# Performance work log

Measured on AMD Instinct MI355X. Metric: run time of the kernel, lower is better.

Reference implementation:

```python
import jax, jax.numpy as jnp
import numpy as np
import math

B, T, D, H, FFN_DIM, SE_HID = 16, 1024, 512, 8, 2048, 256
EPS = 1e-5  # torch LayerNorm default


def layer_norm(x, g, b):
    mu = jnp.mean(x, axis=-1, keepdims=True)
    var = jnp.mean((x - mu) ** 2, axis=-1, keepdims=True)
    return (x - mu) * jax.lax.rsqrt(var + EPS) * g + b


def setup_inputs() -> dict:
    key = jax.random.key(0)
    ks = jax.random.split(key, 8)
    s = 0.02
    return {
        "x": jax.random.normal(ks[0], (B, T, D), dtype=jnp.float32),
        "wq": jax.random.normal(ks[1], (D, D), dtype=jnp.float32) * s,
        "wk": jax.random.normal(ks[2], (D, D), dtype=jnp.float32) * s,
        "wv": jax.random.normal(ks[3], (D, D), dtype=jnp.float32) * s,
        "ln1_g": jnp.ones((D,), jnp.float32),
        "ln1_b": jnp.zeros((D,), jnp.float32),
        "se_w1": jax.random.normal(ks[4], (T, SE_HID), dtype=jnp.float32) * s,
        "se_w2": jax.random.normal(ks[5], (SE_HID, T), dtype=jnp.float32) * s,
        "ffn_g": jnp.ones((D,), jnp.float32),
        "ffn_b": jnp.zeros((D,), jnp.float32),
        "w1": jax.random.normal(ks[6], (D, FFN_DIM), dtype=jnp.float32) * s,
        "b1": jnp.zeros((FFN_DIM,), jnp.float32),
        "w2": jax.random.normal(ks[7], (FFN_DIM, D), dtype=jnp.float32) * s,
        "b2": jnp.zeros((D,), jnp.float32),
    }


def _forward(x, wq, wk, wv, ln1_g, ln1_b, se_w1, se_w2, ffn_g, ffn_b, w1, b1, w2, b2):
    # --- SE gate over the sequence axis: squeeze over feature dim D ---
    y = jnp.mean(x, axis=-1)                       # (B, T)
    gate = jax.nn.sigmoid(jax.nn.relu(y @ se_w1) @ se_w2)  # (B, T)
    x = x + x * gate[..., None]

    d = D // H
    n = layer_norm(x, ln1_g, ln1_b)
    q = (n @ wq).reshape(B, T, H, d)
    k = (n @ wk).reshape(B, T, H, d)
    v = (n @ wv).reshape(B, T, H, d)
    attn = jnp.einsum('bnhd,bmhd->bnmh', q, k) / math.sqrt(d)
    w = jax.nn.softmax(attn, axis=2)               # softmax over key dim m
    x = x + jnp.einsum('bnmh,bmhd->bnhd', w, v).reshape(B, T, D)

    # --- FFN (pre-norm, exact GELU as nn.GELU default) ---
    n2 = layer_norm(x, ffn_g, ffn_b)
    h = jax.nn.gelu(n2 @ w1 + b1, approximate=False)
    return x + (h @ w2 + b2)


def reference(x, wq, wk, wv, ln1_g, ln1_b, se_w1, se_w2, ffn_g, ffn_b, w1, b1, w2, b2):
    return _forward(x, wq, wk, wv, ln1_g, ln1_b, se_w1, se_w2, ffn_g, ffn_b, w1, b1, w2, b2)
```

## Files before the change

kernel.cpp:

```cpp
#include <hip/hip_runtime.h>

typedef unsigned int uint32;

using bf16x8 = __attribute__((ext_vector_type(8))) short;
using f32x4  = __attribute__((ext_vector_type(4))) float;

#define B_  16
#define T_  1024
#define D_  512
#define H_  8
#define HD_ 64
#define FFN_ 2048
#define SEH_ 256
#define EPS_ 1e-5f
#define PS_ 80

__device__ __forceinline__ ushort f2bf(float f) {
  uint32 x = __float_as_uint(f);
  return (ushort)((x + 0x7fffu + ((x >> 16) & 1u)) >> 16);
}
__device__ __forceinline__ float bf2f(ushort u) {
  return __uint_as_float(((uint32)u) << 16);
}
__device__ __forceinline__ float gelu_fast(float v) {
  float u = v * (0.7978845608f + 0.0356774081f * v * v);
  float e = __expf(2.0f * u);
  float t = 1.0f - 2.0f * __builtin_amdgcn_rcpf(e + 1.0f);
  return 0.5f * v * (1.0f + t);
}

__global__ __launch_bounds__(256) void cast_transpose_all_k(
    const float* __restrict__ wq, const float* __restrict__ wk,
    const float* __restrict__ wv, const float* __restrict__ w1,
    const float* __restrict__ w2, ushort* __restrict__ wqkvT,
    ushort* __restrict__ w1T, ushort* __restrict__ w2T) {
  __shared__ float tile[32][33];
  int bid = blockIdx.x;
  const float* W; ushort* WT; int K, N, bk, bn;
  if (bid < 768) {
    int w = bid >> 8, r = bid & 255;
    W = (w == 0) ? wq : (w == 1) ? wk : wv;
    WT = wqkvT + (size_t)w * 512 * 512;
    K = 512; N = 512; bk = (r >> 4) * 32; bn = (r & 15) * 32;
  } else if (bid < 1792) {
    int r = bid - 768;
    W = w1; WT = w1T; K = 512; N = 2048; bk = (r >> 6) * 32; bn = (r & 63) * 32;
  } else {
    int r = bid - 1792;
    W = w2; WT = w2T; K = 2048; N = 512; bk = (r >> 4) * 32; bn = (r & 15) * 32;
  }
  int lx = threadIdx.x & 31;
  int ly = threadIdx.x >> 5;
  #pragma unroll
  for (int i = ly; i < 32; i += 8)
    tile[i][lx] = W[(size_t)(bk + i) * N + bn + lx];
  __syncthreads();
  #pragma unroll
  for (int i = ly; i < 32; i += 8)
    WT[(size_t)(bn + i) * K + bk + lx] = f2bf(tile[lx][i]);
}

__global__ __launch_bounds__(256) void se_rowmean_k(const float* __restrict__ x,
                                                    float* __restrict__ y) {
  int row  = blockIdx.x * 4 + (threadIdx.x >> 6);
  int lane = threadIdx.x & 63;
  const float4* p = (const float4*)(x + (size_t)row * D_);
  float4 a = p[lane * 2];
  float4 b = p[lane * 2 + 1];
  float s = a.x + a.y + a.z + a.w + b.x + b.y + b.z + b.w;
  #pragma unroll
  for (int m = 1; m < 64; m <<= 1) s += __shfl_xor(s, m);
  if (lane == 0) y[row] = s * (1.0f / D_);
}

__global__ __launch_bounds__(256) void se_mlp1_k(const float* __restrict__ y,
                                                 const float* __restrict__ w1,
                                                 float* __restrict__ z) {
  __shared__ float yb[T_];
  __shared__ float part[8][32];
  int b = blockIdx.x, jt = blockIdx.y;
  int tid = threadIdx.x;
  #pragma unroll
  for (int i = 0; i < 4; i++) yb[tid + i * 256] = y[(size_t)b * T_ + tid + i * 256];
  __syncthreads();
  int tj = tid & 31, tk = tid >> 5;
  int j = jt * 32 + tj;
  const float* wp = w1 + (size_t)(tk * 128) * SEH_ + j;
  const float* yp = yb + tk * 128;
  float a0 = 0.f, a1 = 0.f, a2 = 0.f, a3 = 0.f;
  #pragma unroll
  for (int t = 0; t < 128; t += 4) {
    a0 += yp[t]     * wp[(t)     * SEH_];
    a1 += yp[t + 1] * wp[(t + 1) * SEH_];
    a2 += yp[t + 2] * wp[(t + 2) * SEH_];
    a3 += yp[t + 3] * wp[(t + 3) * SEH_];
  }
  part[tk][tj] = (a0 + a1) + (a2 + a3);
  __syncthreads();
  if (tid < 32) {
    float s = 0.f;
    #pragma unroll
    for (int k = 0; k < 8; k++) s += part[k][tid];
    z[(size_t)b * SEH_ + jt * 32 + tid] = fmaxf(s, 0.f);
  }
}

__global__ __launch_bounds__(256) void se_mlp2_k(const float* __restrict__ z,
                                                 const float* __restrict__ w2,
                                                 float* __restrict__ gate) {
  __shared__ float zb[SEH_];
  __shared__ float part[2][128];
  int b = blockIdx.x, bt = blockIdx.y;
  int tid = threadIdx.x;
  zb[tid & 255] = z[(size_t)b * SEH_ + (tid & 255)];
  __syncthreads();
  int tt = tid & 127, tk = tid >> 7;
  int t = bt * 128 + tt;
  const float* wp = w2 + (size_t)(tk * 128) * T_ + t;
  const float* zp = zb + tk * 128;
  float a0 = 0.f, a1 = 0.f, a2 = 0.f, a3 = 0.f;
  #pragma unroll
  for (int j = 0; j < 128; j += 4) {
    a0 += zp[j]     * wp[(j)     * T_];
    a1 += zp[j + 1] * wp[(j + 1) * T_];
    a2 += zp[j + 2] * wp[(j + 2) * T_];
    a3 += zp[j + 3] * wp[(j + 3) * T_];
  }
  part[tk][tt] = (a0 + a1) + (a2 + a3);
  __syncthreads();
  if (tid < 128) {
    float s = part[0][tid] + part[1][tid];
    gate[(size_t)b * T_ + bt * 128 + tid] = 1.0f / (1.0f + __expf(-s));
  }
}

__global__ __launch_bounds__(256) void gate_ln1_k(
    const float* __restrict__ x, const float* __restrict__ gate,
    const float* __restrict__ g, const float* __restrict__ beta,
    float* __restrict__ x1, ushort* __restrict__ nbuf) {
  int rid  = blockIdx.x * 4 + (threadIdx.x >> 6);
  int lane = threadIdx.x & 63;
  const float4* xr = (const float4*)(x + (size_t)rid * D_);
  float4 a = xr[lane * 2];
  float4 b = xr[lane * 2 + 1];
  float gv = 1.0f + gate[rid];
  a.x *= gv; a.y *= gv; a.z *= gv; a.w *= gv;
  b.x *= gv; b.y *= gv; b.z *= gv; b.w *= gv;
  float4* x1r = (float4*)(x1 + (size_t)rid * D_);
  x1r[lane * 2]     = a;
  x1r[lane * 2 + 1] = b;
  float s  = a.x + a.y + a.z + a.w + b.x + b.y + b.z + b.w;
  float ss = a.x*a.x + a.y*a.y + a.z*a.z + a.w*a.w + b.x*b.x + b.y*b.y + b.z*b.z + b.w*b.w;
  #pragma unroll
  for (int m = 1; m < 64; m <<= 1) { s += __shfl_xor(s, m); ss += __shfl_xor(ss, m); }
  float mu   = s * (1.0f / D_);
  float var  = ss * (1.0f / D_) - mu * mu;
  float rstd = rsqrtf(var + EPS_);
  const float4* gp = (const float4*)g;
  const float4* bp = (const float4*)beta;
  float4 g0 = gp[lane * 2], g1 = gp[lane * 2 + 1];
  float4 b0 = bp[lane * 2], b1 = bp[lane * 2 + 1];
  union { uint4 v; ushort u[8]; } pk;
  pk.u[0] = f2bf((a.x - mu) * rstd * g0.x + b0.x);
  pk.u[1] = f2bf((a.y - mu) * rstd * g0.y + b0.y);
  pk.u[2] = f2bf((a.z - mu) * rstd * g0.z + b0.z);
  pk.u[3] = f2bf((a.w - mu) * rstd * g0.w + b0.w);
  pk.u[4] = f2bf((b.x - mu) * rstd * g1.x + b1.x);
  pk.u[5] = f2bf((b.y - mu) * rstd * g1.y + b1.y);
  pk.u[6] = f2bf((b.z - mu) * rstd * g1.z + b1.z);
  pk.u[7] = f2bf((b.w - mu) * rstd * g1.w + b1.w);
  *(uint4*)(nbuf + (size_t)rid * D_ + lane * 8) = pk.v;
}

__global__ __launch_bounds__(256) void ln2_k(
    const float* __restrict__ x2, const float* __restrict__ g,
    const float* __restrict__ beta, ushort* __restrict__ nbuf) {
  int rid  = blockIdx.x * 4 + (threadIdx.x >> 6);
  int lane = threadIdx.x & 63;
  const float4* xr = (const float4*)(x2 + (size_t)rid * D_);
  float4 a = xr[lane * 2];
  float4 b = xr[lane * 2 + 1];
  float s  = a.x + a.y + a.z + a.w + b.x + b.y + b.z + b.w;
  float ss = a.x*a.x + a.y*a.y + a.z*a.z + a.w*a.w + b.x*b.x + b.y*b.y + b.z*b.z + b.w*b.w;
  #pragma unroll
  for (int m = 1; m < 64; m <<= 1) { s += __shfl_xor(s, m); ss += __shfl_xor(ss, m); }
  float mu   = s * (1.0f / D_);
  float var  = ss * (1.0f / D_) - mu * mu;
  float rstd = rsqrtf(var + EPS_);
  const float4* gp = (const float4*)g;
  const float4* bp = (const float4*)beta;
  float4 g0 = gp[lane * 2], g1 = gp[lane * 2 + 1];
  float4 b0 = bp[lane * 2], b1 = bp[lane * 2 + 1];
  union { uint4 v; ushort u[8]; } pk;
  pk.u[0] = f2bf((a.x - mu) * rstd * g0.x + b0.x);
  pk.u[1] = f2bf((a.y - mu) * rstd * g0.y + b0.y);
  pk.u[2] = f2bf((a.z - mu) * rstd * g0.z + b0.z);
  pk.u[3] = f2bf((a.w - mu) * rstd * g0.w + b0.w);
  pk.u[4] = f2bf((b.x - mu) * rstd * g1.x + b1.x);
  pk.u[5] = f2bf((b.y - mu) * rstd * g1.y + b1.y);
  pk.u[6] = f2bf((b.z - mu) * rstd * g1.z + b1.z);
  pk.u[7] = f2bf((b.w - mu) * rstd * g1.w + b1.w);
  *(uint4*)(nbuf + (size_t)rid * D_ + lane * 8) = pk.v;
}

__global__ __launch_bounds__(256) void gemm128_k(
    const ushort* __restrict__ A, const ushort* __restrict__ BT,
    int M, int N, int K,
    const float* __restrict__ bias, const float* __restrict__ resid,
    ushort* __restrict__ outB, ushort* __restrict__ outB2,
    ushort* __restrict__ vTout, float* __restrict__ outF, int epi) {
  __shared__ ushort As[128 * 32];
  __shared__ ushort Bs[128 * 32];
  int tid  = threadIdx.x;
  int wave = tid >> 6;
  int lane = tid & 63;
  int quad = lane >> 4;
  int l15  = lane & 15;
  int wm   = wave >> 1;
  int wn   = wave & 1;
  int m0 = blockIdx.x * 128;
  int n0 = blockIdx.y * 128;

  f32x4 acc[4][4];
  #pragma unroll
  for (int mt = 0; mt < 4; mt++)
    #pragma unroll
    for (int nt = 0; nt < 4; nt++) acc[mt][nt] = (f32x4){0.f, 0.f, 0.f, 0.f};

  int lrow = lane >> 2;
  int lcol = (lane & 3) * 8;

  const ushort* Ag = A  + (size_t)(m0 + wave * 32 + lrow) * K + lcol;
  const ushort* Bg = BT + (size_t)(n0 + wave * 32 + lrow) * K + lcol;
  ushort* AsW = As + (wave * 32) * 32;
  ushort* BsW = Bs + (wave * 32) * 32;

  for (int kk = 0; kk < K; kk += 32) {
    __builtin_amdgcn_global_load_lds(
        (const __attribute__((address_space(1))) void*)(Ag + kk),
        (__attribute__((address_space(3))) void*)AsW, 16, 0, 0);
    __builtin_amdgcn_global_load_lds(
        (const __attribute__((address_space(1))) void*)(Ag + kk + 16 * (size_t)K),
        (__attribute__((address_space(3))) void*)(AsW + 16 * 32), 16, 0, 0);
    __builtin_amdgcn_global_load_lds(
        (const __attribute__((address_space(1))) void*)(Bg + kk),
        (__attribute__((address_space(3))) void*)BsW, 16, 0, 0);
    __builtin_amdgcn_global_load_lds(
        (const __attribute__((address_space(1))) void*)(Bg + kk + 16 * (size_t)K),
        (__attribute__((address_space(3))) void*)(BsW + 16 * 32), 16, 0, 0);
    __syncthreads();
    bf16x8 af[4], bfr[4];
    #pragma unroll
    for (int mt = 0; mt < 4; mt++)
      af[mt] = *(const bf16x8*)(As + (wm * 64 + mt * 16 + l15) * 32 + quad * 8);
    #pragma unroll
    for (int nt = 0; nt < 4; nt++)
      bfr[nt] = *(const bf16x8*)(Bs + (wn * 64 + nt * 16 + l15) * 32 + quad * 8);
    #pragma unroll
    for (int mt = 0; mt < 4; mt++)
      #pragma unroll
      for (int nt = 0; nt < 4; nt++)
        acc[mt][nt] = __builtin_amdgcn_mfma_f32_16x16x32_bf16(af[mt], bfr[nt], acc[mt][nt], 0, 0, 0);
    __syncthreads();
  }

  if (epi == 1) {
    #pragma unroll
    for (int nt = 0; nt < 4; nt++) {
      int n = n0 + wn * 64 + nt * 16 + l15;
      float bv = bias[n];
      #pragma unroll
      for (int mt = 0; mt < 4; mt++) {
        #pragma unroll
        for (int r = 0; r < 4; r++) {
          int m = m0 + wm * 64 + mt * 16 + quad * 4 + r;
          outB[(size_t)m * N + n] = f2bf(gelu_fast(acc[mt][nt][r] + bv));
        }
      }
    }
  } else if (epi == 2) {
    #pragma unroll
    for (int nt = 0; nt < 4; nt++) {
      int n = n0 + wn * 64 + nt * 16 + l15;
      float bv = bias[n];
      #pragma unroll
      for (int mt = 0; mt < 4; mt++) {
        #pragma unroll
        for (int r = 0; r < 4; r++) {
          int m = m0 + wm * 64 + mt * 16 + quad * 4 + r;
          size_t idx = (size_t)m * N + n;
          outF[idx] = acc[mt][nt][r] + bv + resid[idx];
        }
      }
    }
  } else {
    if (n0 < 1024) {
      ushort* dst = (n0 < 512) ? outB : outB2;
      float scl = (n0 < 512) ? 0.125f : 1.0f;
      int nb = n0 & 511;
      #pragma unroll
      for (int nt = 0; nt < 4; nt++) {
        int n = nb + wn * 64 + nt * 16 + l15;
        #pragma unroll
        for (int mt = 0; mt < 4; mt++) {
          #pragma unroll
          for (int r = 0; r < 4; r++) {
            int m = m0 + wm * 64 + mt * 16 + quad * 4 + r;
            dst[(size_t)m * 512 + n] = f2bf(acc[mt][nt][r] * scl);
          }
        }
      }
    } else {
      #pragma unroll
      for (int nt = 0; nt < 4; nt++) {
        int n = (n0 - 1024) + wn * 64 + nt * 16 + l15;
        int h = n >> 6, d = n & 63;
        #pragma unroll
        for (int mt = 0; mt < 4; mt++) {
          int mb = m0 + wm * 64 + mt * 16 + quad * 4;
          int bb = mb >> 10, t = mb & 1023;
          ushort4 pk;
          pk.x = f2bf(acc[mt][nt][0]);
          pk.y = f2bf(acc[mt][nt][1]);
          pk.z = f2bf(acc[mt][nt][2]);
          pk.w = f2bf(acc[mt][nt][3]);
          *(ushort4*)(vTout + (((size_t)bb * 8 + h) * 64 + d) * 1024 + t) = pk;
        }
      }
    }
  }
}

__global__ __launch_bounds__(256) void attn_k(
    const ushort* __restrict__ q, const ushort* __restrict__ k,
    const ushort* __restrict__ vT, const float* __restrict__ x1,
    float* __restrict__ out) {
  __shared__ ushort Ks[64 * PS_];
  __shared__ ushort Vs[64 * PS_];
  __shared__ ushort Ps[64 * PS_];
  int blk = blockIdx.x;
  int qt = blk & 15;
  int h  = (blk >> 4) & 7;
  int b  = blk >> 7;
  int t0 = qt * 64;
  int tid  = threadIdx.x;
  int wave = tid >> 6;
  int lane = tid & 63;
  int quad = lane >> 4;
  int l15  = lane & 15;

  const ushort* qp = q + ((size_t)(b * T_ + t0 + wave * 16 + l15)) * D_ + h * HD_;
  bf16x8 aq0 = *(const bf16x8*)(qp + quad * 8);
  bf16x8 aq1 = *(const bf16x8*)(qp + 32 + quad * 8);

  int srow = tid >> 2;
  int scol = (tid & 3) * 16;

  float l_part[4] = {0.f, 0.f, 0.f, 0.f};
  f32x4 o_acc[4];
  #pragma unroll
  for (int dt = 0; dt < 4; dt++) o_acc[dt] = (f32x4){0.f, 0.f, 0.f, 0.f};

  const ushort* vTb = vT + ((size_t)(b * 8 + h) * 64 + srow) * 1024 + scol;

  for (int kt = 0; kt < 16; kt++) {
    size_t kgbase = ((size_t)(b * T_ + kt * 64 + srow)) * D_ + h * HD_ + scol;
    uint4 ku0 = *(const uint4*)(k + kgbase);
    uint4 ku1 = *(const uint4*)(k + kgbase + 8);
    const ushort* vp = vTb + kt * 64;
    uint4 vv0 = *(const uint4*)(vp);
    uint4 vv1 = *(const uint4*)(vp + 8);

    __syncthreads();

    *(uint4*)(Ks + srow * PS_ + scol)     = ku0;
    *(uint4*)(Ks + srow * PS_ + scol + 8) = ku1;
    *(uint4*)(Vs + srow * PS_ + scol)     = vv0;
    *(uint4*)(Vs + srow * PS_ + scol + 8) = vv1;

    __syncthreads();

    f32x4 s_acc[4];
    #pragma unroll
    for (int nt = 0; nt < 4; nt++) {
      s_acc[nt] = (f32x4){0.f, 0.f, 0.f, 0.f};
      bf16x8 bk0 = *(const bf16x8*)(Ks + (nt * 16 + l15) * PS_ + quad * 8);
      bf16x8 bk1 = *(const bf16x8*)(Ks + (nt * 16 + l15) * PS_ + 32 + quad * 8);
      s_acc[nt] = __builtin_amdgcn_mfma_f32_16x16x32_bf16(aq0, bk0, s_acc[nt], 0, 0, 0);
      s_acc[nt] = __builtin_amdgcn_mfma_f32_16x16x32_bf16(aq1, bk1, s_acc[nt], 0, 0, 0);
    }

    #pragma unroll
    for (int nt = 0; nt < 4; nt++) {
      int pcol = nt * 16 + l15;
      #pragma unroll
      for (int r = 0; r < 4; r++) {
        float p = __expf(s_acc[nt][r]);
        l_part[r] += p;
        Ps[(wave * 16 + quad * 4 + r) * PS_ + pcol] = f2bf(p);
      }
    }

    __syncthreads();

    bf16x8 ap0 = *(const bf16x8*)(Ps + (wave * 16 + l15) * PS_ + quad * 8);
    bf16x8 ap1 = *(const bf16x8*)(Ps + (wave * 16 + l15) * PS_ + 32 + quad * 8);
    #pragma unroll
    for (int dt = 0; dt < 4; dt++) {
      bf16x8 bv0 = *(const bf16x8*)(Vs + (dt * 16 + l15) * PS_ + quad * 8);
      bf16x8 bv1 = *(const bf16x8*)(Vs + (dt * 16 + l15) * PS_ + 32 + quad * 8);
      o_acc[dt] = __builtin_amdgcn_mfma_f32_16x16x32_bf16(ap0, bv0, o_acc[dt], 0, 0, 0);
      o_acc[dt] = __builtin_amdgcn_mfma_f32_16x16x32_bf16(ap1, bv1, o_acc[dt], 0, 0, 0);
    }
  }

  #pragma unroll
  for (int r = 0; r < 4; r++) {
    float l = l_part[r];
    l += __shfl_xor(l, 1);
    l += __shfl_xor(l, 2);
    l += __shfl_xor(l, 4);
    l += __shfl_xor(l, 8);
    float inv = 1.0f / l;
    int qrow = t0 + wave * 16 + quad * 4 + r;
    size_t base = ((size_t)(b * T_ + qrow)) * D_ + h * HD_;
    #pragma unroll
    for (int dt = 0; dt < 4; dt++) {
      size_t idx = base + dt * 16 + l15;
      out[idx] = x1[idx] + o_acc[dt][r] * inv;
    }
  }
}

extern "C" void kernel_launch(void* const* d_in, const int* in_sizes, int n_in,
                              void* d_out, int out_size, void* d_ws, size_t ws_size,
                              hipStream_t stream) {
  (void)in_sizes; (void)n_in; (void)out_size; (void)ws_size;
  const float* x     = (const float*)d_in[0];
  const float* wq    = (const float*)d_in[1];
  const float* wk    = (const float*)d_in[2];
  const float* wv    = (const float*)d_in[3];
  const float* ln1_g = (const float*)d_in[4];
  const float* ln1_b = (const float*)d_in[5];
  const float* se_w1 = (const float*)d_in[6];
  const float* se_w2 = (const float*)d_in[7];
  const float* ffn_g = (const float*)d_in[8];
  const float* ffn_b = (const float*)d_in[9];
  const float* w1    = (const float*)d_in[10];
  const float* b1    = (const float*)d_in[11];
  const float* w2    = (const float*)d_in[12];
  const float* b2    = (const float*)d_in[13];
  float* out = (float*)d_out;
  char* ws = (char*)d_ws;

  constexpr size_t X1_OFF   = 0;
  constexpr size_t N_OFF    = 33554432;
  constexpr size_t Q_OFF    = 50331648;
  constexpr size_t K_OFF    = 67108864;
  constexpr size_t V_OFF    = 83886080;
  constexpr size_t H_OFF    = 50331648;
  constexpr size_t WQKV_OFF = 117440512;
  constexpr size_t W1T_OFF  = 119013376;
  constexpr size_t W2T_OFF  = 121110528;
  constexpr size_t Y_OFF    = 123207680;
  constexpr size_t Z_OFF    = 123273216;
  constexpr size_t GATE_OFF = 123289600;

  float*  x1    = (float*)(ws + X1_OFF);
  ushort* nbuf  = (ushort*)(ws + N_OFF);
  ushort* qb    = (ushort*)(ws + Q_OFF);
  ushort* kb    = (ushort*)(ws + K_OFF);
  ushort* vT    = (ushort*)(ws + V_OFF);
  ushort* hb    = (ushort*)(ws + H_OFF);
  ushort* wqkvT = (ushort*)(ws + WQKV_OFF);
  ushort* w1T   = (ushort*)(ws + W1T_OFF);
  ushort* w2T   = (ushort*)(ws + W2T_OFF);
  float*  yv    = (float*)(ws + Y_OFF);
  float*  zv    = (float*)(ws + Z_OFF);
  float*  gate  = (float*)(ws + GATE_OFF);

  const int M = B_ * T_;

  cast_transpose_all_k<<<2816, 256, 0, stream>>>(wq, wk, wv, w1, w2, wqkvT, w1T, w2T);

  se_rowmean_k<<<M / 4, 256, 0, stream>>>(x, yv);
  se_mlp1_k<<<dim3(B_, 8), 256, 0, stream>>>(yv, se_w1, zv);
  se_mlp2_k<<<dim3(B_, 8), 256, 0, stream>>>(zv, se_w2, gate);

  gate_ln1_k<<<M / 4, 256, 0, stream>>>(x, gate, ln1_g, ln1_b, x1, nbuf);

  gemm128_k<<<dim3(M / 128, 1536 / 128), 256, 0, stream>>>(
      nbuf, wqkvT, M, 1536, D_, nullptr, nullptr, qb, kb, vT, nullptr, 3);

  attn_k<<<B_ * H_ * (T_ / 64), 256, 0, stream>>>(qb, kb, vT, x1, out);

  ln2_k<<<M / 4, 256, 0, stream>>>(out, ffn_g, ffn_b, nbuf);

  gemm128_k<<<dim3(M / 128, FFN_ / 128), 256, 0, stream>>>(
      nbuf, w1T, M, FFN_, D_, b1, nullptr, hb, nullptr, nullptr, nullptr, 1);
  gemm128_k<<<dim3(M / 128, D_ / 128), 256, 0, stream>>>(
      hb, w2T, M, D_, FFN_, b2, out, nullptr, nullptr, nullptr, out, 2);
}
```

Before: 382.8 us.

## Process 128 queries per attention block and reorder GEMM grid for reuse

The attention kernel now handles two 64-query sub-tiles per block. Each staged K/V tile in shared memory therefore feeds twice as much MFMA work, and the grid is halved. The barrier between writing and reading the P tile is dropped, because each wave reads only the rows it wrote itself. The GEMM grid is transposed so consecutive blocks walk along N and share the same A row-tile in cache. The cost is more registers and double the P shared-memory buffer, which could lower occupancy.

Result: no change. 378.6 us (-1.1%).

```diff
diff --git a/kernel.cpp b/kernel.cpp
--- a/kernel.cpp
+++ b/kernel.cpp
@@ -218,8 +218,8 @@
   int l15  = lane & 15;
   int wm   = wave >> 1;
   int wn   = wave & 1;
-  int m0 = blockIdx.x * 128;
-  int n0 = blockIdx.y * 128;
+  int n0 = blockIdx.x * 128;
+  int m0 = blockIdx.y * 128;
 
   f32x4 acc[4][4];
   #pragma unroll
@@ -337,29 +337,35 @@
     float* __restrict__ out) {
   __shared__ ushort Ks[64 * PS_];
   __shared__ ushort Vs[64 * PS_];
-  __shared__ ushort Ps[64 * PS_];
+  __shared__ ushort Ps[128 * PS_];
   int blk = blockIdx.x;
-  int qt = blk & 15;
-  int h  = (blk >> 4) & 7;
-  int b  = blk >> 7;
-  int t0 = qt * 64;
+  int qt = blk & 7;
+  int h  = (blk >> 3) & 7;
+  int b  = blk >> 6;
+  int t0 = qt * 128;
   int tid  = threadIdx.x;
   int wave = tid >> 6;
   int lane = tid & 63;
   int quad = lane >> 4;
   int l15  = lane & 15;
 
-  const ushort* qp = q + ((size_t)(b * T_ + t0 + wave * 16 + l15)) * D_ + h * HD_;
-  bf16x8 aq0 = *(const bf16x8*)(qp + quad * 8);
-  bf16x8 aq1 = *(const bf16x8*)(qp + 32 + quad * 8);
+  const ushort* qp0 = q + ((size_t)(b * T_ + t0 + wave * 16 + l15)) * D_ + h * HD_;
+  const ushort* qp1 = qp0 + (size_t)64 * D_;
+  bf16x8 aq0 = *(const bf16x8*)(qp0 + quad * 8);
+  bf16x8 aq1 = *(const bf16x8*)(qp0 + 32 + quad * 8);
+  bf16x8 aq2 = *(const bf16x8*)(qp1 + quad * 8);
+  bf16x8 aq3 = *(const bf16x8*)(qp1 + 32 + quad * 8);
 
   int srow = tid >> 2;
   int scol = (tid & 3) * 16;
 
-  float l_part[4] = {0.f, 0.f, 0.f, 0.f};
-  f32x4 o_acc[4];
-  #pragma unroll
-  for (int dt = 0; dt < 4; dt++) o_acc[dt] = (f32x4){0.f, 0.f, 0.f, 0.f};
+  float l_part[2][4] = {{0.f, 0.f, 0.f, 0.f}, {0.f, 0.f, 0.f, 0.f}};
+  f32x4 o0[4], o1[4];
+  #pragma unroll
+  for (int dt = 0; dt < 4; dt++) {
+    o0[dt] = (f32x4){0.f, 0.f, 0.f, 0.f};
+    o1[dt] = (f32x4){0.f, 0.f, 0.f, 0.f};
+  }
 
   const ushort* vTb = vT + ((size_t)(b * 8 + h) * 64 + srow) * 1024 + scol;
 
@@ -380,54 +386,66 @@
 
     __syncthreads();
 
-    f32x4 s_acc[4];
+    f32x4 s0[4], s1[4];
     #pragma unroll
     for (int nt = 0; nt < 4; nt++) {
-      s_acc[nt] = (f32x4){0.f, 0.f, 0.f, 0.f};
       bf16x8 bk0 = *(const bf16x8*)(Ks + (nt * 16 + l15) * PS_ + quad * 8);
       bf16x8 bk1 = *(const bf16x8*)(Ks + (nt * 16 + l15) * PS_ + 32 + quad * 8);
-      s_acc[nt] = __builtin_amdgcn_mfma_f32_16x16x32_bf16(aq0, bk0, s_acc[nt], 0, 0, 0);
-      s_acc[nt] = __builtin_amdgcn_mfma_f32_16x16x32_bf16(aq1, bk1, s_acc[nt], 0, 0, 0);
+      f32x4 z = (f32x4){0.f, 0.f, 0.f, 0.f};
+      s0[nt] = __builtin_amdgcn_mfma_f32_16x16x32_bf16(aq0, bk0, z, 0, 0, 0);
+      s0[nt] = __builtin_amdgcn_mfma_f32_16x16x32_bf16(aq1, bk1, s0[nt], 0, 0, 0);
+      s1[nt] = __builtin_amdgcn_mfma_f32_16x16x32_bf16(aq2, bk0, z, 0, 0, 0);
+      s1[nt] = __builtin_amdgcn_mfma_f32_16x16x32_bf16(aq3, bk1, s1[nt], 0, 0, 0);
     }
 
     #pragma unroll
     for (int nt = 0; nt < 4; nt++) {
       int pcol = nt * 16 + l15;
+      int prow0 = (wave * 16 + quad * 4) * PS_ + pcol;
       #pragma unroll
       for (int r = 0; r < 4; r++) {
-        float p = __expf(s_acc[nt][r]);
-        l_part[r] += p;
-        Ps[(wave * 16 + quad * 4 + r) * PS_ + pcol] = f2bf(p);
+        float p0 = __expf(s0[nt][r]);
+        float p1 = __expf(s1[nt][r]);
+        l_part[0][r] += p0;
+        l_part[1][r] += p1;
+        Ps[prow0 + r * PS_]            = f2bf(p0);
+        Ps[prow0 + (64 + r) * PS_]     = f2bf(p1);
       }
     }
-
-    __syncthreads();
 
     bf16x8 ap0 = *(const bf16x8*)(Ps + (wave * 16 + l15) * PS_ + quad * 8);
     bf16x8 ap1 = *(const bf16x8*)(Ps + (wave * 16 + l15) * PS_ + 32 + quad * 8);
+    bf16x8 ap2 = *(const bf16x8*)(Ps + (64 + wave * 16 + l15) * PS_ + quad * 8);
+    bf16x8 ap3 = *(const bf16x8*)(Ps + (64 + wave * 16 + l15) * PS_ + 32 + quad * 8);
     #pragma unroll
     for (int dt = 0; dt < 4; dt++) {
       bf16x8 bv0 = *(const bf16x8*)(Vs + (dt * 16 + l15) * PS_ + quad * 8);
       bf16x8 bv1 = *(const bf16x8*)(Vs + (dt * 16 + l15) * PS_ + 32 + quad * 8);
-      o_acc[dt] = __builtin_amdgcn_mfma_f32_16x16x32_bf16(ap0, bv0, o_acc[dt], 0, 0, 0);
-      o_acc[dt] = __builtin_amdgcn_mfma_f32_16x16x32_bf16(ap1, bv1, o_acc[dt], 0, 0, 0);
-    }
-  }
-
-  #pragma unroll
-  for (int r = 0; r < 4; r++) {
-    float l = l_part[r];
-    l += __shfl_xor(l, 1);
-    l += __shfl_xor(l, 2);
-    l += __shfl_xor(l, 4);
-    l += __shfl_xor(l, 8);
-    float inv = 1.0f / l;
-    int qrow = t0 + wave * 16 + quad * 4 + r;
-    size_t base = ((size_t)(b * T_ + qrow)) * D_ + h * HD_;
-    #pragma unroll
-    for (int dt = 0; dt < 4; dt++) {
-      size_t idx = base + dt * 16 + l15;
-      out[idx] = x1[idx] + o_acc[dt][r] * inv;
+      o0[dt] = __builtin_amdgcn_mfma_f32_16x16x32_bf16(ap0, bv0, o0[dt], 0, 0, 0);
+      o0[dt] = __builtin_amdgcn_mfma_f32_16x16x32_bf16(ap1, bv1, o0[dt], 0, 0, 0);
+      o1[dt] = __builtin_amdgcn_mfma_f32_16x16x32_bf16(ap2, bv0, o1[dt], 0, 0, 0);
+      o1[dt] = __builtin_amdgcn_mfma_f32_16x16x32_bf16(ap3, bv1, o1[dt], 0, 0, 0);
+    }
+  }
+
+  #pragma unroll
+  for (int s = 0; s < 2; s++) {
+    f32x4* oo = s ? o1 : o0;
+    #pragma unroll
+    for (int r = 0; r < 4; r++) {
+      float l = l_part[s][r];
+      l += __shfl_xor(l, 1);
+      l += __shfl_xor(l, 2);
+      l += __shfl_xor(l, 4);
+      l += __shfl_xor(l, 8);
+      float inv = 1.0f / l;
+      int qrow = t0 + s * 64 + wave * 16 + quad * 4 + r;
+      size_t base = ((size_t)(b * T_ + qrow)) * D_ + h * HD_;
+      #pragma unroll
+      for (int dt = 0; dt < 4; dt++) {
+        size_t idx = base + dt * 16 + l15;
+        out[idx] = x1[idx] + oo[dt][r] * inv;
+      }
     }
   }
 }
@@ -489,15 +507,15 @@
 
   gate_ln1_k<<<M / 4, 256, 0, stream>>>(x, gate, ln1_g, ln1_b, x1, nbuf);
 
-  gemm128_k<<<dim3(M / 128, 1536 / 128), 256, 0, stream>>>(
+  gemm128_k<<<dim3(1536 / 128, M / 128), 256, 0, stream>>>(
       nbuf, wqkvT, M, 1536, D_, nullptr, nullptr, qb, kb, vT, nullptr, 3);
 
-  attn_k<<<B_ * H_ * (T_ / 64), 256, 0, stream>>>(qb, kb, vT, x1, out);
+  attn_k<<<B_ * H_ * (T_ / 128), 256, 0, stream>>>(qb, kb, vT, x1, out);
 
   ln2_k<<<M / 4, 256, 0, stream>>>(out, ffn_g, ffn_b, nbuf);
 
-  gemm128_k<<<dim3(M / 128, FFN_ / 128), 256, 0, stream>>>(
+  gemm128_k<<<dim3(FFN_ / 128, M / 128), 256, 0, stream>>>(
       nbuf, w1T, M, FFN_, D_, b1, nullptr, hb, nullptr, nullptr, nullptr, 1);
-  gemm128_k<<<dim3(M / 128, D_ / 128), 256, 0, stream>>>(
+  gemm128_k<<<dim3(D_ / 128, M / 128), 256, 0, stream>>>(
       hb, w2T, M, D_, FFN_, b2, out, nullptr, nullptr, nullptr, out, 2);
 }
```
